# Performance work log

Hardware: AMD Instinct MI355X
Metric: run time of the kernel (lower is better)

Reference implementation:

```python
import jax, jax.numpy as jnp
import numpy as np

VOCAB = 30000
N_NODES = 10000
N_EDGES = 160000
D = 1024


def setup_inputs() -> dict:
    key = jax.random.key(0)
    ks = jax.random.split(key, 10)
    s = 1.0 / np.sqrt(D)
    return {
        "node": jax.random.randint(ks[0], (N_NODES,), 0, VOCAB),
        "src": jax.random.randint(ks[1], (N_EDGES,), 0, N_NODES),
        "dst": jax.random.randint(ks[2], (N_EDGES,), 0, N_NODES),
        "emb": jax.random.normal(ks[3], (VOCAB, D), jnp.float32),
        "W1_self": jax.random.uniform(ks[4], (D, D), jnp.float32, -s, s),
        "W1_neigh": jax.random.uniform(ks[5], (D, D), jnp.float32, -s, s),
        "b1": jax.random.uniform(ks[6], (D,), jnp.float32, -s, s),
        "W2_self": jax.random.uniform(ks[7], (D, D), jnp.float32, -s, s),
        "W2_neigh": jax.random.uniform(ks[8], (D, D), jnp.float32, -s, s),
        "b2": jax.random.uniform(ks[9], (D,), jnp.float32, -s, s),
    }


def _sage_conv(h, src, dst, W_self, W_neigh, b):
    # DGL SAGEConv 'mean': mean over in-neighbors (src -> dst), 0 for isolated dst
    n = h.shape[0]
    deg = jax.ops.segment_sum(jnp.ones((src.shape[0],), h.dtype), dst, num_segments=n)
    agg = jax.ops.segment_sum(h[src], dst, num_segments=n)  # [n, D]
    h_neigh = agg / jnp.maximum(deg, 1.0)[:, None]
    # rst = fc_self(h) + fc_neigh(h_neigh); fc_self has no bias in DGL
    return h @ W_self + h_neigh @ W_neigh + b


def reference(node, src, dst, emb, W1_self, W1_neigh, b1, W2_self, W2_neigh, b2):
    x = emb[node]  # [N_NODES, D] embedding lookup
    h = jax.nn.relu(_sage_conv(x, src, dst, W1_self, W1_neigh, b1))
    return _sage_conv(h, src, dst, W2_self, W2_neigh, b2)
```

## Files before the change

kernel.cpp:

```cpp
#include <hip/hip_runtime.h>
#include <hip/hip_bf16.h>

#define N_NODES 10000
#define N_EDGES 160000
#define DD 1024
#define KCAT 2048
#define MPAD 10240
#define MTILES 79

typedef __attribute__((ext_vector_type(8))) __bf16 bf16x8;
typedef __attribute__((ext_vector_type(4))) __bf16 bf16x4;
typedef __attribute__((ext_vector_type(4))) float f32x4;

__device__ inline void gload_lds16(const void* g, void* l) {
  __builtin_amdgcn_global_load_lds((const __attribute__((address_space(1))) void*)g,
                                   (__attribute__((address_space(3))) void*)l, 16, 0, 0);
}

__global__ __launch_bounds__(256) void k_hist(const int* __restrict__ dst,
                                              int* __restrict__ deg) {
  int e = blockIdx.x * 256 + threadIdx.x;
  if (e < N_EDGES) atomicAdd(&deg[dst[e]], 1);
}

__global__ __launch_bounds__(1024) void k_scan(const int* __restrict__ deg,
                                               int* __restrict__ off) {
  __shared__ int sh[1024];
  __shared__ int carry_s;
  int t = threadIdx.x;
  if (t == 0) carry_s = 0;
  for (int base = 0; base < N_NODES; base += 1024) {
    int v = (base + t < N_NODES) ? deg[base + t] : 0;
    __syncthreads();
    sh[t] = v;
    __syncthreads();
    int c0 = carry_s;
    for (int s = 1; s < 1024; s <<= 1) {
      int x = (t >= s) ? sh[t - s] : 0;
      __syncthreads();
      sh[t] += x;
      __syncthreads();
    }
    if (base + t < N_NODES) off[base + t] = c0 + sh[t] - v;
    int tot = sh[1023];
    __syncthreads();
    if (t == 0) carry_s = c0 + tot;
  }
  __syncthreads();
  if (t == 0) off[N_NODES] = carry_s;
}

__global__ __launch_bounds__(256) void k_fill(const int* __restrict__ src,
                                              const int* __restrict__ dst,
                                              const int* __restrict__ off,
                                              int* __restrict__ cursor,
                                              int* __restrict__ eidx) {
  int e = blockIdx.x * 256 + threadIdx.x;
  if (e < N_EDGES) {
    int d = dst[e];
    int pos = atomicAdd(&cursor[d], 1);
    eidx[off[d] + pos] = src[e];
  }
}

__global__ __launch_bounds__(256) void k_embed(const int* __restrict__ node,
                                               const float* __restrict__ emb,
                                               __bf16* __restrict__ xcat) {
  int i = blockIdx.x;
  int t = threadIdx.x;
  float4 v = ((const float4*)(emb + (size_t)node[i] * DD))[t];
  bf16x4 o;
  o[0] = (__bf16)v.x; o[1] = (__bf16)v.y; o[2] = (__bf16)v.z; o[3] = (__bf16)v.w;
  *(bf16x4*)(xcat + (size_t)i * KCAT + t * 4) = o;
}

__global__ __launch_bounds__(256) void k_wconv(const float* __restrict__ Ws,
                                               const float* __restrict__ Wn,
                                               __bf16* __restrict__ Wt) {
  __shared__ float tile[32][33];
  int k0 = blockIdx.x * 32;
  int c0 = blockIdx.y * 32;
  for (int i = threadIdx.y; i < 32; i += 8) {
    int k = k0 + i, c = c0 + threadIdx.x;
    float v = (k < DD) ? Ws[(size_t)k * DD + c] : Wn[(size_t)(k - DD) * DD + c];
    tile[i][threadIdx.x] = v;
  }
  __syncthreads();
  for (int i = threadIdx.y; i < 32; i += 8) {
    int c = c0 + i, k = k0 + threadIdx.x;
    Wt[(size_t)c * KCAT + k] = (__bf16)tile[threadIdx.x][i];
  }
}

__global__ __launch_bounds__(256) void k_agg(__bf16* __restrict__ buf,
                                             const int* __restrict__ off,
                                             const int* __restrict__ eidx) {
  int d = blockIdx.x;
  int t = threadIdx.x;
  int s = off[d], e = off[d + 1];
  float a0 = 0.f, a1 = 0.f, a2 = 0.f, a3 = 0.f;
  for (int i = s; i < e; ++i) {
    int r = eidx[i];
    bf16x4 v = *(const bf16x4*)(buf + (size_t)r * KCAT + t * 4);
    a0 += (float)v[0]; a1 += (float)v[1]; a2 += (float)v[2]; a3 += (float)v[3];
  }
  float inv = 1.0f / fmaxf((float)(e - s), 1.0f);
  bf16x4 o;
  o[0] = (__bf16)(a0 * inv); o[1] = (__bf16)(a1 * inv);
  o[2] = (__bf16)(a2 * inv); o[3] = (__bf16)(a3 * inv);
  *(bf16x4*)(buf + (size_t)d * KCAT + DD + t * 4) = o;
}

template <int MODE>
__global__ __launch_bounds__(256) void k_gemm(const __bf16* __restrict__ A,
                                              const __bf16* __restrict__ Bt,
                                              const float* __restrict__ bias,
                                              float* __restrict__ Cf,
                                              __bf16* __restrict__ Cb,
                                              int Mreal) {
  __shared__ uint4 smemq[2048];
  char* As = (char*)smemq;
  char* Bs = As + 16384;
  const int tid  = threadIdx.x;
  const int lane = tid & 63;
  const int w    = tid >> 6;
  const int wr   = w >> 1, wc = w & 1;
  const int m0   = blockIdx.x * 128;
  const int n0   = blockIdx.y * 128;

  f32x4 acc[4][4];
#pragma unroll
  for (int m = 0; m < 4; ++m)
#pragma unroll
    for (int n = 0; n < 4; ++n) acc[m][n] = f32x4{0.f, 0.f, 0.f, 0.f};

  int sr[4], sk[4];
#pragma unroll
  for (int i = 0; i < 4; ++i) {
    int G = (4 * w + i) * 64 + lane;
    int E = G ^ ((G >> 3) & 7);
    sr[i] = E >> 3;
    sk[i] = (E & 7) * 8;
  }

  for (int kt = 0; kt < KCAT; kt += 64) {
    __syncthreads();
#pragma unroll
    for (int i = 0; i < 4; ++i) {
      gload_lds16(A + (size_t)(m0 + sr[i]) * KCAT + (kt + sk[i]), As + (4 * w + i) * 1024);
      gload_lds16(Bt + (size_t)(n0 + sr[i]) * KCAT + (kt + sk[i]), Bs + (4 * w + i) * 1024);
    }
    __syncthreads();
#pragma unroll
    for (int kk = 0; kk < 64; kk += 32) {
      const int koff = kk + ((lane >> 4) * 8);
      bf16x8 af[4], bfr[4];
#pragma unroll
      for (int m = 0; m < 4; ++m) {
        int r = wr * 64 + m * 16 + (lane & 15);
        int byte = ((r * 64 + koff) * 2) ^ ((r & 7) << 4);
        af[m] = *(const bf16x8*)(As + byte);
      }
#pragma unroll
      for (int n = 0; n < 4; ++n) {
        int c = wc * 64 + n * 16 + (lane & 15);
        int byte = ((c * 64 + koff) * 2) ^ ((c & 7) << 4);
        bfr[n] = *(const bf16x8*)(Bs + byte);
      }
#pragma unroll
      for (int m = 0; m < 4; ++m)
#pragma unroll
        for (int n = 0; n < 4; ++n)
          acc[m][n] = __builtin_amdgcn_mfma_f32_16x16x32_bf16(af[m], bfr[n], acc[m][n], 0, 0, 0);
    }
  }

  const int rb = m0 + wr * 64;
  const int cb = n0 + wc * 64;
#pragma unroll
  for (int m = 0; m < 4; ++m) {
#pragma unroll
    for (int n = 0; n < 4; ++n) {
      int c = cb + n * 16 + (lane & 15);
      float bv = bias[c];
#pragma unroll
      for (int j = 0; j < 4; ++j) {
        int r = rb + m * 16 + (lane >> 4) * 4 + j;
        if (r < Mreal) {
          float v = acc[m][n][j] + bv;
          if constexpr (MODE == 1) {
            v = fmaxf(v, 0.f);
            Cb[(size_t)r * KCAT + c] = (__bf16)v;
          } else {
            Cf[(size_t)r * DD + c] = v;
          }
        }
      }
    }
  }
}

extern "C" void kernel_launch(void* const* d_in, const int* in_sizes, int n_in,
                              void* d_out, int out_size, void* d_ws, size_t ws_size,
                              hipStream_t stream) {
  const int*   node = (const int*)d_in[0];
  const int*   srcv = (const int*)d_in[1];
  const int*   dstv = (const int*)d_in[2];
  const float* emb  = (const float*)d_in[3];
  const float* W1s  = (const float*)d_in[4];
  const float* W1n  = (const float*)d_in[5];
  const float* b1   = (const float*)d_in[6];
  const float* W2s  = (const float*)d_in[7];
  const float* W2n  = (const float*)d_in[8];
  const float* b2   = (const float*)d_in[9];
  float* out = (float*)d_out;

  char* ws = (char*)d_ws;
  __bf16* xcat = (__bf16*)ws; ws += (size_t)MPAD * KCAT * 2;
  __bf16* hcat = (__bf16*)ws; ws += (size_t)MPAD * KCAT * 2;
  __bf16* Wt1  = (__bf16*)ws; ws += (size_t)DD * KCAT * 2;
  __bf16* Wt2  = (__bf16*)ws; ws += (size_t)DD * KCAT * 2;
  int* deg    = (int*)ws; ws += 40960;
  int* cursor = (int*)ws; ws += 40960;
  int* off    = (int*)ws; ws += 40960;
  int* eidx   = (int*)ws; ws += (size_t)N_EDGES * 4;

  hipMemsetAsync(deg, 0, N_NODES * sizeof(int), stream);
  hipMemsetAsync(cursor, 0, N_NODES * sizeof(int), stream);

  k_hist<<<(N_EDGES + 255) / 256, 256, 0, stream>>>(dstv, deg);
  k_scan<<<1, 1024, 0, stream>>>(deg, off);
  k_fill<<<(N_EDGES + 255) / 256, 256, 0, stream>>>(srcv, dstv, off, cursor, eidx);

  k_embed<<<N_NODES, 256, 0, stream>>>(node, emb, xcat);
  k_wconv<<<dim3(64, 32), dim3(32, 8), 0, stream>>>(W1s, W1n, Wt1);
  k_wconv<<<dim3(64, 32), dim3(32, 8), 0, stream>>>(W2s, W2n, Wt2);

  k_agg<<<N_NODES, 256, 0, stream>>>(xcat, off, eidx);
  k_gemm<1><<<dim3(MTILES, 8), 256, 0, stream>>>(xcat, Wt1, b1, nullptr, hcat, N_NODES);

  k_agg<<<N_NODES, 256, 0, stream>>>(hcat, off, eidx);
  k_gemm<0><<<dim3(MTILES, 8), 256, 0, stream>>>(hcat, Wt2, b2, out, nullptr, N_NODES);
}
```

Measured before the change: 509.0 us.

## Double-buffer GEMM LDS, swizzle block order, warp-per-node aggregation, faster scan

```diff
diff --git a/kernel.cpp b/kernel.cpp
--- a/kernel.cpp
+++ b/kernel.cpp
@@ -7,6 +7,8 @@
 #define KCAT 2048
 #define MPAD 10240
 #define MTILES 79
+#define NTILES 8
+#define NBLK (MTILES * NTILES)
 
 typedef __attribute__((ext_vector_type(8))) __bf16 bf16x8;
 typedef __attribute__((ext_vector_type(4))) __bf16 bf16x4;
@@ -25,29 +27,40 @@
 
 __global__ __launch_bounds__(1024) void k_scan(const int* __restrict__ deg,
                                                int* __restrict__ off) {
-  __shared__ int sh[1024];
-  __shared__ int carry_s;
   int t = threadIdx.x;
-  if (t == 0) carry_s = 0;
-  for (int base = 0; base < N_NODES; base += 1024) {
-    int v = (base + t < N_NODES) ? deg[base + t] : 0;
-    __syncthreads();
-    sh[t] = v;
-    __syncthreads();
-    int c0 = carry_s;
-    for (int s = 1; s < 1024; s <<= 1) {
-      int x = (t >= s) ? sh[t - s] : 0;
-      __syncthreads();
-      sh[t] += x;
-      __syncthreads();
-    }
-    if (base + t < N_NODES) off[base + t] = c0 + sh[t] - v;
-    int tot = sh[1023];
-    __syncthreads();
-    if (t == 0) carry_s = c0 + tot;
-  }
-  __syncthreads();
-  if (t == 0) off[N_NODES] = carry_s;
+  int base_i = t * 10;
+  int loc[10];
+  int sum = 0;
+#pragma unroll
+  for (int j = 0; j < 10; ++j) {
+    int idx = base_i + j;
+    int v = (idx < N_NODES) ? deg[idx] : 0;
+    loc[j] = sum;
+    sum += v;
+  }
+  int lane = t & 63, w = t >> 6;
+  int inc = sum;
+#pragma unroll
+  for (int d = 1; d < 64; d <<= 1) {
+    int y = __shfl_up(inc, d);
+    if (lane >= d) inc += y;
+  }
+  __shared__ int wtot[16];
+  __shared__ int wpre[16];
+  if (lane == 63) wtot[w] = inc;
+  __syncthreads();
+  if (t == 0) {
+    int c = 0;
+    for (int k = 0; k < 16; ++k) { wpre[k] = c; c += wtot[k]; }
+    off[N_NODES] = c;
+  }
+  __syncthreads();
+  int tbase = wpre[w] + (inc - sum);
+#pragma unroll
+  for (int j = 0; j < 10; ++j) {
+    int idx = base_i + j;
+    if (idx < N_NODES) off[idx] = tbase + loc[j];
+  }
 }
 
 __global__ __launch_bounds__(256) void k_fill(const int* __restrict__ src,
@@ -95,38 +108,65 @@
 __global__ __launch_bounds__(256) void k_agg(__bf16* __restrict__ buf,
                                              const int* __restrict__ off,
                                              const int* __restrict__ eidx) {
-  int d = blockIdx.x;
-  int t = threadIdx.x;
-  int s = off[d], e = off[d + 1];
-  float a0 = 0.f, a1 = 0.f, a2 = 0.f, a3 = 0.f;
-  for (int i = s; i < e; ++i) {
-    int r = eidx[i];
-    bf16x4 v = *(const bf16x4*)(buf + (size_t)r * KCAT + t * 4);
-    a0 += (float)v[0]; a1 += (float)v[1]; a2 += (float)v[2]; a3 += (float)v[3];
+  int wid = blockIdx.x * 4 + (threadIdx.x >> 6);
+  if (wid >= N_NODES) return;
+  int lane = threadIdx.x & 63;
+  int s = off[wid], e = off[wid + 1];
+  size_t col = (size_t)lane * 16;
+  float acc0[16], acc1[16];
+#pragma unroll
+  for (int j = 0; j < 16; ++j) { acc0[j] = 0.f; acc1[j] = 0.f; }
+  int i = s;
+  for (; i + 2 <= e; i += 2) {
+    const __bf16* r0 = buf + (size_t)eidx[i] * KCAT + col;
+    const __bf16* r1 = buf + (size_t)eidx[i + 1] * KCAT + col;
+    bf16x8 u0 = *(const bf16x8*)r0;
+    bf16x8 u1 = *(const bf16x8*)(r0 + 8);
+    bf16x8 v0 = *(const bf16x8*)r1;
+    bf16x8 v1 = *(const bf16x8*)(r1 + 8);
+#pragma unroll
+    for (int j = 0; j < 8; ++j) {
+      acc0[j]     += (float)u0[j];
+      acc0[8 + j] += (float)u1[j];
+      acc1[j]     += (float)v0[j];
+      acc1[8 + j] += (float)v1[j];
+    }
+  }
+  if (i < e) {
+    const __bf16* r0 = buf + (size_t)eidx[i] * KCAT + col;
+    bf16x8 u0 = *(const bf16x8*)r0;
+    bf16x8 u1 = *(const bf16x8*)(r0 + 8);
+#pragma unroll
+    for (int j = 0; j < 8; ++j) { acc0[j] += (float)u0[j]; acc0[8 + j] += (float)u1[j]; }
   }
   float inv = 1.0f / fmaxf((float)(e - s), 1.0f);
-  bf16x4 o;
-  o[0] = (__bf16)(a0 * inv); o[1] = (__bf16)(a1 * inv);
-  o[2] = (__bf16)(a2 * inv); o[3] = (__bf16)(a3 * inv);
-  *(bf16x4*)(buf + (size_t)d * KCAT + DD + t * 4) = o;
+  bf16x8 o0, o1;
+#pragma unroll
+  for (int j = 0; j < 8; ++j) {
+    o0[j] = (__bf16)((acc0[j] + acc1[j]) * inv);
+    o1[j] = (__bf16)((acc0[8 + j] + acc1[8 + j]) * inv);
+  }
+  __bf16* dstp = buf + (size_t)wid * KCAT + DD + col;
+  *(bf16x8*)dstp = o0;
+  *(bf16x8*)(dstp + 8) = o1;
 }
 
 template <int MODE>
-__global__ __launch_bounds__(256) void k_gemm(const __bf16* __restrict__ A,
-                                              const __bf16* __restrict__ Bt,
-                                              const float* __restrict__ bias,
-                                              float* __restrict__ Cf,
-                                              __bf16* __restrict__ Cb,
-                                              int Mreal) {
-  __shared__ uint4 smemq[2048];
-  char* As = (char*)smemq;
-  char* Bs = As + 16384;
+__global__ __launch_bounds__(256, 2) void k_gemm(const __bf16* __restrict__ A,
+                                                 const __bf16* __restrict__ Bt,
+                                                 const float* __restrict__ bias,
+                                                 float* __restrict__ Cf,
+                                                 __bf16* __restrict__ Cb,
+                                                 int Mreal) {
+  __shared__ char smem[65536];
   const int tid  = threadIdx.x;
   const int lane = tid & 63;
   const int w    = tid >> 6;
   const int wr   = w >> 1, wc = w & 1;
-  const int m0   = blockIdx.x * 128;
-  const int n0   = blockIdx.y * 128;
+  const int b  = blockIdx.x;
+  const int l  = (b & 7) * MTILES + (b >> 3);
+  const int m0 = (l >> 3) * 128;
+  const int n0 = (l & 7) * 128;
 
   f32x4 acc[4][4];
 #pragma unroll
@@ -143,14 +183,19 @@
     sk[i] = (E & 7) * 8;
   }
 
-  for (int kt = 0; kt < KCAT; kt += 64) {
-    __syncthreads();
+  auto stage = [&](int buf, int kt) {
+    char* As = smem + buf * 32768;
+    char* Bs = As + 16384;
 #pragma unroll
     for (int i = 0; i < 4; ++i) {
       gload_lds16(A + (size_t)(m0 + sr[i]) * KCAT + (kt + sk[i]), As + (4 * w + i) * 1024);
       gload_lds16(Bt + (size_t)(n0 + sr[i]) * KCAT + (kt + sk[i]), Bs + (4 * w + i) * 1024);
     }
-    __syncthreads();
+  };
+
+  auto compute = [&](int buf) {
+    char* As = smem + buf * 32768;
+    char* Bs = As + 16384;
 #pragma unroll
     for (int kk = 0; kk < 64; kk += 32) {
       const int koff = kk + ((lane >> 4) * 8);
@@ -173,6 +218,16 @@
         for (int n = 0; n < 4; ++n)
           acc[m][n] = __builtin_amdgcn_mfma_f32_16x16x32_bf16(af[m], bfr[n], acc[m][n], 0, 0, 0);
     }
+  };
+
+  stage(0, 0);
+  __syncthreads();
+  int cur = 0;
+  for (int kt = 0; kt < KCAT; kt += 64) {
+    if (kt + 64 < KCAT) stage(cur ^ 1, kt + 64);
+    compute(cur);
+    __syncthreads();
+    cur ^= 1;
   }
 
   const int rb = m0 + wr * 64;
@@ -236,9 +291,9 @@
   k_wconv<<<dim3(64, 32), dim3(32, 8), 0, stream>>>(W1s, W1n, Wt1);
   k_wconv<<<dim3(64, 32), dim3(32, 8), 0, stream>>>(W2s, W2n, Wt2);
 
-  k_agg<<<N_NODES, 256, 0, stream>>>(xcat, off, eidx);
-  k_gemm<1><<<dim3(MTILES, 8), 256, 0, stream>>>(xcat, Wt1, b1, nullptr, hcat, N_NODES);
-
-  k_agg<<<N_NODES, 256, 0, stream>>>(hcat, off, eidx);
-  k_gemm<0><<<dim3(MTILES, 8), 256, 0, stream>>>(hcat, Wt2, b2, out, nullptr, N_NODES);
-}
+  k_agg<<<2500, 256, 0, stream>>>(xcat, off, eidx);
+  k_gemm<1><<<NBLK, 256, 0, stream>>>(xcat, Wt1, b1, nullptr, hcat, N_NODES);
+
+  k_agg<<<2500, 256, 0, stream>>>(hcat, off, eidx);
+  k_gemm<0><<<NBLK, 256, 0, stream>>>(hcat, Wt2, b2, out, nullptr, N_NODES);
+}
```

Result: faster. 457.5 us (-10.1%).
